# Kernel optimization log

Measured on AMD Instinct MI355X. Metric: run time of the kernel, lower is better.

## Reference

```python
import jax, jax.numpy as jnp
import numpy as np

N_NODES = 200000
N_FRAGS = 50000
N_EDGES = 400000
HDIM = 128
VOCAB = 800


def setup_inputs() -> dict:
    key = jax.random.key(0)
    ks = jax.random.split(key, 9)
    x = jax.random.normal(ks[0], (N_NODES, HDIM), dtype=jnp.float32)
    fragments = jax.random.uniform(ks[1], (N_FRAGS, VOCAB), dtype=jnp.float32)
    emb_table = jax.random.normal(ks[2], (VOCAB, HDIM), dtype=jnp.float32)
    W_f = jax.random.normal(ks[3], (HDIM, HDIM), dtype=jnp.float32) / np.sqrt(HDIM)
    b_f = jax.random.normal(ks[4], (HDIM,), dtype=jnp.float32) * 0.01
    W_s = jax.random.normal(ks[5], (2 * HDIM, HDIM), dtype=jnp.float32) / np.sqrt(2 * HDIM)
    b_s = jax.random.normal(ks[6], (HDIM,), dtype=jnp.float32) * 0.01
    row = jax.random.randint(ks[7], (N_EDGES,), 0, N_NODES, dtype=jnp.int32)
    col = jax.random.randint(ks[8], (N_EDGES,), 0, N_FRAGS, dtype=jnp.int32)
    return {"x": x, "fragments": fragments, "emb_table": emb_table,
            "W_f": W_f, "b_f": b_f, "W_s": W_s, "b_s": b_s,
            "row": row, "col": col}


def _scatter_mean(vals, idx, num_segments):
    s = jax.ops.segment_sum(vals, idx, num_segments=num_segments)
    cnt = jax.ops.segment_sum(jnp.ones((vals.shape[0], 1), vals.dtype), idx,
                              num_segments=num_segments)
    return s / jnp.maximum(cnt, 1.0)


def reference(x, fragments, emb_table, W_f, b_f, W_s, b_s, row, col):
    N, H = x.shape
    F = fragments.shape[0]
    # gather node feats along memberships, mean-pool per fragment: [F, H]
    substructure_x = _scatter_mean(x[row], col, F)
    # fragment type embedding branch
    frag_ids = jnp.argmax(fragments, axis=1)            # [F]
    fragments_emb = emb_table[frag_ids] @ W_f + b_f      # [F, H]
    substructure_x = jnp.concatenate([substructure_x, fragments_emb], axis=1)  # [F, 2H]
    fragment_emb = substructure_x @ W_s + b_s            # [F, H]
    # gather fragment embeddings back to memberships, mean-pool per node: [N, H]
    return _scatter_mean(fragment_emb[col], row, N)
```

## Files before the change

### kernel.cpp

```cpp
#include <hip/hip_runtime.h>

#define HDIM 128
#define VOCAB 800
#define FB 16
#define NB 64
#define TILE 1024
#define TILE_N 512

typedef float f4 __attribute__((ext_vector_type(4)));

#define ACCB(a, h) { \
    a.x += __uint_as_float(h.x << 16); \
    a.y += __uint_as_float(h.x & 0xffff0000u); \
    a.z += __uint_as_float(h.y << 16); \
    a.w += __uint_as_float(h.y & 0xffff0000u); }

static __device__ __forceinline__ unsigned short f2bf(float f) {
    unsigned int u = __float_as_uint(f);
    return (unsigned short)((u + 0x7fffu + ((u >> 16) & 1u)) >> 16);
}

__global__ void k_prep(const float* __restrict__ emb, const float* __restrict__ W_f,
                       const float* __restrict__ W_s, const float* __restrict__ b_f,
                       const float* __restrict__ b_s, float* __restrict__ E2,
                       float* __restrict__ bfs) {
    __shared__ float e[HDIM], t1[HDIM];
    int j = threadIdx.x;
    int v = blockIdx.x;
    if (v < VOCAB) {
        e[j] = emb[(size_t)v * HDIM + j];
        __syncthreads();
        float a = 0.f;
        for (int k = 0; k < HDIM; ++k)
            a = fmaf(e[k], W_f[k * HDIM + j], a);
        t1[j] = a;
        __syncthreads();
        float b = 0.f;
        for (int k = 0; k < HDIM; ++k)
            b = fmaf(t1[k], W_s[(HDIM + k) * HDIM + j], b);
        E2[(size_t)v * HDIM + j] = b;
    } else {
        e[j] = b_f[j];
        __syncthreads();
        float b = b_s[j];
        for (int k = 0; k < HDIM; ++k)
            b = fmaf(e[k], W_s[(HDIM + k) * HDIM + j], b);
        bfs[j] = b;
    }
}

__global__ void k_amc(const float* __restrict__ frags, int* __restrict__ frag_id,
                      const float* __restrict__ x, unsigned short* __restrict__ xb,
                      const int* __restrict__ row, const int* __restrict__ col,
                      int* __restrict__ cntr, int* __restrict__ cntc) {
    int b = blockIdx.x, t = threadIdx.x;
    if (b < 12500) {
        int wave = b * 4 + (t >> 6);
        int lane = t & 63;
        const f4* r = reinterpret_cast<const f4*>(frags + (size_t)wave * VOCAB);
        float best = -1e30f;
        int bidx = 0;
        for (int i = lane; i < VOCAB / 4; i += 64) {
            f4 v = __builtin_nontemporal_load(r + i);
            int base = i * 4;
            if (v.x > best) { best = v.x; bidx = base + 0; }
            if (v.y > best) { best = v.y; bidx = base + 1; }
            if (v.z > best) { best = v.z; bidx = base + 2; }
            if (v.w > best) { best = v.w; bidx = base + 3; }
        }
        for (int off = 32; off > 0; off >>= 1) {
            float ov = __shfl_xor(best, off, 64);
            int   oi = __shfl_xor(bidx, off, 64);
            if (ov > best || (ov == best && oi < bidx)) { best = ov; bidx = oi; }
        }
        if (lane == 0) frag_id[wave] = bidx;
    } else if (b < 12891) {
        int i = (b - 12500) * 256 + t;
        if (i < 100000) {
            int4 r4 = reinterpret_cast<const int4*>(row)[i];
            int4 c4 = reinterpret_cast<const int4*>(col)[i];
            atomicAdd(&cntr[r4.x], 1); atomicAdd(&cntr[r4.y], 1);
            atomicAdd(&cntr[r4.z], 1); atomicAdd(&cntr[r4.w], 1);
            atomicAdd(&cntc[c4.x], 1); atomicAdd(&cntc[c4.y], 1);
            atomicAdd(&cntc[c4.z], 1); atomicAdd(&cntc[c4.w], 1);
        }
    } else {
        size_t i = (size_t)(b - 12891) * 256 + t;
        const f4* xp = reinterpret_cast<const f4*>(x);
        f4 v0 = __builtin_nontemporal_load(xp + 2 * i);
        f4 v1 = __builtin_nontemporal_load(xp + 2 * i + 1);
        uint4 o;
        o.x = (unsigned)f2bf(v0.x) | ((unsigned)f2bf(v0.y) << 16);
        o.y = (unsigned)f2bf(v0.z) | ((unsigned)f2bf(v0.w) << 16);
        o.z = (unsigned)f2bf(v1.x) | ((unsigned)f2bf(v1.y) << 16);
        o.w = (unsigned)f2bf(v1.z) | ((unsigned)f2bf(v1.w) << 16);
        *reinterpret_cast<uint4*>(xb + i * 8) = o;
    }
}

__global__ void k_bsum2(const int* __restrict__ cntc, const int* __restrict__ cntr,
                        int* __restrict__ bsc, int* __restrict__ bsr, int NBC, int F, int N) {
    __shared__ int s[256];
    int t = threadIdx.x;
    const int* cnt;
    int* bsum;
    int bb, L;
    if ((int)blockIdx.x < NBC) { cnt = cntc; bsum = bsc; bb = blockIdx.x; L = F; }
    else                       { cnt = cntr; bsum = bsr; bb = blockIdx.x - NBC; L = N; }
    int i = bb * 256 + t;
    s[t] = (i < L) ? cnt[i] : 0;
    __syncthreads();
    for (int o = 128; o > 0; o >>= 1) {
        if (t < o) s[t] += s[t + o];
        __syncthreads();
    }
    if (t == 0) bsum[bb] = s[0];
}

__global__ void k_scan2(int* __restrict__ bsc, int* __restrict__ bsr, int nbc, int nbr) {
    __shared__ int s[1024];
    int* bsum = (blockIdx.x == 0) ? bsc : bsr;
    int nb    = (blockIdx.x == 0) ? nbc : nbr;
    int t = threadIdx.x;
    int v = (t < nb) ? bsum[t] : 0;
    s[t] = v;
    __syncthreads();
    for (int o = 1; o < 1024; o <<= 1) {
        int a = (t >= o) ? s[t - o] : 0;
        __syncthreads();
        s[t] += a;
        __syncthreads();
    }
    if (t < nb) bsum[t] = s[t] - v;
}

__global__ void k_base2(const int* __restrict__ cntc, const int* __restrict__ cntr,
                        const int* __restrict__ bsc, const int* __restrict__ bsr,
                        int* __restrict__ basec, int* __restrict__ baser,
                        int NBC, int F, int N) {
    __shared__ int s[256];
    int t = threadIdx.x;
    const int *cnt, *bsum;
    int* base;
    int bb, L;
    if ((int)blockIdx.x < NBC) { cnt = cntc; bsum = bsc; base = basec; bb = blockIdx.x; L = F; }
    else                       { cnt = cntr; bsum = bsr; base = baser; bb = blockIdx.x - NBC; L = N; }
    int i = bb * 256 + t;
    int v = (i < L) ? cnt[i] : 0;
    s[t] = v;
    __syncthreads();
    for (int o = 1; o < 256; o <<= 1) {
        int a = (t >= o) ? s[t - o] : 0;
        __syncthreads();
        s[t] += a;
        __syncthreads();
    }
    if (i < L) base[i] = bsum[bb] + s[t] - v;
}

__global__ void k_place(const int* __restrict__ row, const int* __restrict__ col,
                        int* __restrict__ basec, int* __restrict__ baser,
                        int* __restrict__ payc, int* __restrict__ payr, int E) {
    int e = blockIdx.x * 256 + threadIdx.x;
    if (e >= E) return;
    int r = row[e], c = col[e];
    int pc = atomicAdd(&basec[c], 1);
    payc[pc] = r;
    int pr = atomicAdd(&baser[r], 1);
    payr[pr] = c;
}

__global__ __launch_bounds__(256) void k_frag(
        const unsigned short* __restrict__ xb, const int* __restrict__ basec,
        const int* __restrict__ payc, const int* __restrict__ frag_id,
        const float* __restrict__ W_s, const float* __restrict__ E2,
        const float* __restrict__ bfs, unsigned short* __restrict__ fembb) {
    __shared__ float s[FB][HDIM];
    __shared__ int eidx[TILE];
    __shared__ int cb[FB + 1];
    int t = threadIdx.x;
    int g = t >> 5, l = t & 31;
    int fb = blockIdx.x * FB;
    if (t <= FB) {
        int idx = fb + t - 1;
        cb[t] = (idx < 0) ? 0 : basec[idx];
    }
    __syncthreads();
    int st0 = cb[g],     d0 = cb[g + 1] - cb[g];
    int st1 = cb[8 + g], d1 = cb[9 + g] - cb[8 + g];
    int p0 = cb[0], pend = cb[FB];
    const uint2* x2 = reinterpret_cast<const uint2*>(xb);
    float4 a0A = make_float4(0.f, 0.f, 0.f, 0.f), a0B = a0A, a1A = a0A, a1B = a0A;
    for (int tb = p0; tb < pend; tb += TILE) {
        int nload = min(TILE, pend - tb);
        for (int i = t; i < nload; i += 256) eidx[i] = payc[tb + i];
        __syncthreads();
        int lim = tb + nload;
        int lo0 = max(st0, tb) - tb, hi0 = min(st0 + d0, lim) - tb;
        int lo1 = max(st1, tb) - tb, hi1 = min(st1 + d1, lim) - tb;
        int m = max(hi0 - lo0, hi1 - lo1);
        for (int j = 0; j < m; j += 2) {
            if (lo0 + j < hi0)     { uint2 h = x2[(size_t)eidx[lo0 + j]     * 32 + l]; ACCB(a0A, h); }
            if (lo0 + j + 1 < hi0) { uint2 h = x2[(size_t)eidx[lo0 + j + 1] * 32 + l]; ACCB(a0B, h); }
            if (lo1 + j < hi1)     { uint2 h = x2[(size_t)eidx[lo1 + j]     * 32 + l]; ACCB(a1A, h); }
            if (lo1 + j + 1 < hi1) { uint2 h = x2[(size_t)eidx[lo1 + j + 1] * 32 + l]; ACCB(a1B, h); }
        }
        __syncthreads();
    }
    float inv0 = 1.0f / fmaxf((float)d0, 1.0f);
    float inv1 = 1.0f / fmaxf((float)d1, 1.0f);
    float4 r0, r1;
    r0.x = (a0A.x + a0B.x) * inv0; r0.y = (a0A.y + a0B.y) * inv0;
    r0.z = (a0A.z + a0B.z) * inv0; r0.w = (a0A.w + a0B.w) * inv0;
    r1.x = (a1A.x + a1B.x) * inv1; r1.y = (a1A.y + a1B.y) * inv1;
    r1.z = (a1A.z + a1B.z) * inv1; r1.w = (a1A.w + a1B.w) * inv1;
    *reinterpret_cast<float4*>(&s[g][l * 4]) = r0;
    *reinterpret_cast<float4*>(&s[8 + g][l * 4]) = r1;
    __syncthreads();
    int d = t & 127;
    int fh = t >> 7;
    float bv = bfs[d];
    float acc[8];
#pragma unroll
    for (int f = 0; f < 8; ++f)
        acc[f] = E2[(size_t)frag_id[fb + fh * 8 + f] * HDIM + d] + bv;
    for (int k = 0; k < HDIM; k += 4) {
        float w0 = W_s[(k + 0) * HDIM + d];
        float w1 = W_s[(k + 1) * HDIM + d];
        float w2 = W_s[(k + 2) * HDIM + d];
        float w3 = W_s[(k + 3) * HDIM + d];
#pragma unroll
        for (int f = 0; f < 8; ++f) {
            const float4 sv = *reinterpret_cast<const float4*>(&s[fh * 8 + f][k]);
            acc[f] = fmaf(sv.x, w0, acc[f]);
            acc[f] = fmaf(sv.y, w1, acc[f]);
            acc[f] = fmaf(sv.z, w2, acc[f]);
            acc[f] = fmaf(sv.w, w3, acc[f]);
        }
    }
#pragma unroll
    for (int f = 0; f < 8; ++f)
        fembb[(size_t)(fb + fh * 8 + f) * HDIM + d] = f2bf(acc[f]);
}

__global__ __launch_bounds__(256) void k_node(
        const unsigned short* __restrict__ fembb, const int* __restrict__ baser,
        const int* __restrict__ payr, float* __restrict__ out, int N) {
    __shared__ int eidx[TILE_N];
    __shared__ int cb[NB + 1];
    int t = threadIdx.x;
    int g = t >> 5, l = t & 31;
    int n0 = blockIdx.x * NB;
    if (t <= NB) {
        int idx = n0 + t - 1;
        cb[t] = (idx < 0) ? 0 : baser[idx];
    }
    __syncthreads();
    int st_[8], dg_[8];
    float4 a[8];
#pragma unroll
    for (int i = 0; i < 8; ++i) {
        st_[i] = cb[g * 8 + i];
        dg_[i] = cb[g * 8 + i + 1] - st_[i];
        a[i] = make_float4(0.f, 0.f, 0.f, 0.f);
    }
    int p0 = cb[0], pend = cb[NB];
    const uint2* f2p = reinterpret_cast<const uint2*>(fembb);
    for (int tb = p0; tb < pend; tb += TILE_N) {
        int nload = min(TILE_N, pend - tb);
        for (int i = t; i < nload; i += 256) eidx[i] = payr[tb + i];
        __syncthreads();
        int lim = tb + nload;
        int lo[8], hi[8];
        int m = 0;
#pragma unroll
        for (int i = 0; i < 8; ++i) {
            lo[i] = max(st_[i], tb) - tb;
            hi[i] = min(st_[i] + dg_[i], lim) - tb;
            m = max(m, hi[i] - lo[i]);
        }
        for (int j = 0; j < m; ++j) {
#pragma unroll
            for (int i = 0; i < 8; ++i) {
                if (lo[i] + j < hi[i]) {
                    uint2 h = f2p[(size_t)eidx[lo[i] + j] * 32 + l];
                    ACCB(a[i], h);
                }
            }
        }
        __syncthreads();
    }
    f4* o4 = reinterpret_cast<f4*>(out);
#pragma unroll
    for (int i = 0; i < 8; ++i) {
        float inv = 1.0f / fmaxf((float)dg_[i], 1.0f);
        f4 v;
        v.x = a[i].x * inv; v.y = a[i].y * inv;
        v.z = a[i].z * inv; v.w = a[i].w * inv;
        __builtin_nontemporal_store(v, o4 + (size_t)(n0 + g * 8 + i) * 32 + l);
    }
}

extern "C" void kernel_launch(void* const* d_in, const int* in_sizes, int n_in,
                              void* d_out, int out_size, void* d_ws, size_t ws_size,
                              hipStream_t stream) {
    const float* x         = (const float*)d_in[0];
    const float* fragments = (const float*)d_in[1];
    const float* emb_table = (const float*)d_in[2];
    const float* W_f       = (const float*)d_in[3];
    const float* b_f       = (const float*)d_in[4];
    const float* W_s       = (const float*)d_in[5];
    const float* b_s       = (const float*)d_in[6];
    const int*   row       = (const int*)d_in[7];
    const int*   col       = (const int*)d_in[8];
    float* out = (float*)d_out;

    const int N = 200000, F = 50000, E = 400000;
    const int NBC = (F + 255) / 256;
    const int NBR = (N + 255) / 256;

    unsigned short* xb = (unsigned short*)d_out;

    unsigned short* fembb = (unsigned short*)d_ws;
    int* cntc    = (int*)(fembb + (size_t)F * HDIM);
    int* cntr    = cntc + F;
    int* basec   = cntr + N;
    int* baser   = basec + F;
    int* bsc     = baser + N;
    int* bsr     = bsc + 1024;
    int* payc    = bsr + 1024;
    int* payr    = payc + E;
    int* frag_id = payr + E;
    float* E2    = (float*)(frag_id + F);
    float* bfs   = E2 + VOCAB * HDIM;

    hipMemsetAsync(cntc, 0, (size_t)(F + N) * sizeof(int), stream);

    k_amc<<<12891 + 12500, 256, 0, stream>>>(fragments, frag_id, x, xb, row, col, cntr, cntc);
    k_bsum2<<<NBC + NBR, 256, 0, stream>>>(cntc, cntr, bsc, bsr, NBC, F, N);
    k_scan2<<<2, 1024, 0, stream>>>(bsc, bsr, NBC, NBR);
    k_base2<<<NBC + NBR, 256, 0, stream>>>(cntc, cntr, bsc, bsr, basec, baser, NBC, F, N);
    k_place<<<(E + 255) / 256, 256, 0, stream>>>(row, col, basec, baser, payc, payr, E);
    k_prep<<<VOCAB + 1, HDIM, 0, stream>>>(emb_table, W_f, W_s, b_f, b_s, E2, bfs);
    k_frag<<<F / FB, 256, 0, stream>>>(xb, basec, payc, frag_id, W_s, E2, bfs, fembb);
    k_node<<<N / NB, 256, 0, stream>>>(fembb, baser, payr, out, N);
}
```

Before: 251.0 us.

## Merge CSR builds into one scan, fuse prep into k_amc, widen fragment blocks

Concatenates the column and row count/base/payload arrays so one bsum/scan/base chain serves both CSR builds. It folds the embedding-prep matmuls into the tail blocks of k_amc and vectorizes k_place to int4 loads. It also doubles the fragments per block in k_frag, packing fragment pairs into float2 shared memory for the dense projection. The goal is fewer launches and better W_s reuse, at the cost of more registers per thread and fewer k_frag blocks.

```diff
diff --git a/kernel.cpp b/kernel.cpp
--- a/kernel.cpp
+++ b/kernel.cpp
@@ -2,12 +2,13 @@
 
 #define HDIM 128
 #define VOCAB 800
-#define FB 16
+#define FB 32
 #define NB 64
 #define TILE 1024
 #define TILE_N 512
 
 typedef float f4 __attribute__((ext_vector_type(4)));
+typedef float f2 __attribute__((ext_vector_type(2)));
 
 #define ACCB(a, h) { \
     a.x += __uint_as_float(h.x << 16); \
@@ -20,39 +21,15 @@
     return (unsigned short)((u + 0x7fffu + ((u >> 16) & 1u)) >> 16);
 }
 
-__global__ void k_prep(const float* __restrict__ emb, const float* __restrict__ W_f,
-                       const float* __restrict__ W_s, const float* __restrict__ b_f,
-                       const float* __restrict__ b_s, float* __restrict__ E2,
-                       float* __restrict__ bfs) {
-    __shared__ float e[HDIM], t1[HDIM];
-    int j = threadIdx.x;
-    int v = blockIdx.x;
-    if (v < VOCAB) {
-        e[j] = emb[(size_t)v * HDIM + j];
-        __syncthreads();
-        float a = 0.f;
-        for (int k = 0; k < HDIM; ++k)
-            a = fmaf(e[k], W_f[k * HDIM + j], a);
-        t1[j] = a;
-        __syncthreads();
-        float b = 0.f;
-        for (int k = 0; k < HDIM; ++k)
-            b = fmaf(t1[k], W_s[(HDIM + k) * HDIM + j], b);
-        E2[(size_t)v * HDIM + j] = b;
-    } else {
-        e[j] = b_f[j];
-        __syncthreads();
-        float b = b_s[j];
-        for (int k = 0; k < HDIM; ++k)
-            b = fmaf(e[k], W_s[(HDIM + k) * HDIM + j], b);
-        bfs[j] = b;
-    }
-}
-
 __global__ void k_amc(const float* __restrict__ frags, int* __restrict__ frag_id,
                       const float* __restrict__ x, unsigned short* __restrict__ xb,
                       const int* __restrict__ row, const int* __restrict__ col,
-                      int* __restrict__ cntr, int* __restrict__ cntc) {
+                      int* __restrict__ cnt,
+                      const float* __restrict__ emb, const float* __restrict__ W_f,
+                      const float* __restrict__ W_s, const float* __restrict__ b_f,
+                      const float* __restrict__ b_s, float* __restrict__ E2,
+                      float* __restrict__ bfs, int F) {
+    __shared__ float e[2][HDIM], t1[2][HDIM];
     int b = blockIdx.x, t = threadIdx.x;
     if (b < 12500) {
         int wave = b * 4 + (t >> 6);
@@ -79,12 +56,12 @@
         if (i < 100000) {
             int4 r4 = reinterpret_cast<const int4*>(row)[i];
             int4 c4 = reinterpret_cast<const int4*>(col)[i];
-            atomicAdd(&cntr[r4.x], 1); atomicAdd(&cntr[r4.y], 1);
-            atomicAdd(&cntr[r4.z], 1); atomicAdd(&cntr[r4.w], 1);
-            atomicAdd(&cntc[c4.x], 1); atomicAdd(&cntc[c4.y], 1);
-            atomicAdd(&cntc[c4.z], 1); atomicAdd(&cntc[c4.w], 1);
-        }
-    } else {
+            atomicAdd(&cnt[F + r4.x], 1); atomicAdd(&cnt[F + r4.y], 1);
+            atomicAdd(&cnt[F + r4.z], 1); atomicAdd(&cnt[F + r4.w], 1);
+            atomicAdd(&cnt[c4.x], 1); atomicAdd(&cnt[c4.y], 1);
+            atomicAdd(&cnt[c4.z], 1); atomicAdd(&cnt[c4.w], 1);
+        }
+    } else if (b < 25391) {
         size_t i = (size_t)(b - 12891) * 256 + t;
         const f4* xp = reinterpret_cast<const f4*>(x);
         f4 v0 = __builtin_nontemporal_load(xp + 2 * i);
@@ -95,32 +72,50 @@
         o.z = (unsigned)f2bf(v1.x) | ((unsigned)f2bf(v1.y) << 16);
         o.w = (unsigned)f2bf(v1.z) | ((unsigned)f2bf(v1.w) << 16);
         *reinterpret_cast<uint4*>(xb + i * 8) = o;
-    }
-}
-
-__global__ void k_bsum2(const int* __restrict__ cntc, const int* __restrict__ cntr,
-                        int* __restrict__ bsc, int* __restrict__ bsr, int NBC, int F, int N) {
+    } else {
+        int bp = b - 25391;
+        int j = t & 127, half = t >> 7;
+        if (bp < 400) {
+            int v = bp * 2 + half;
+            e[half][j] = emb[(size_t)v * HDIM + j];
+            __syncthreads();
+            float a = 0.f;
+            for (int k = 0; k < HDIM; ++k)
+                a = fmaf(e[half][k], W_f[k * HDIM + j], a);
+            t1[half][j] = a;
+            __syncthreads();
+            float bb = 0.f;
+            for (int k = 0; k < HDIM; ++k)
+                bb = fmaf(t1[half][k], W_s[(HDIM + k) * HDIM + j], bb);
+            E2[(size_t)v * HDIM + j] = bb;
+        } else {
+            if (half == 0) e[0][j] = b_f[j];
+            __syncthreads();
+            if (half == 0) {
+                float bb = b_s[j];
+                for (int k = 0; k < HDIM; ++k)
+                    bb = fmaf(e[0][k], W_s[(HDIM + k) * HDIM + j], bb);
+                bfs[j] = bb;
+            }
+        }
+    }
+}
+
+__global__ void k_bsum(const int* __restrict__ cnt, int L, int* __restrict__ bsum) {
     __shared__ int s[256];
     int t = threadIdx.x;
-    const int* cnt;
-    int* bsum;
-    int bb, L;
-    if ((int)blockIdx.x < NBC) { cnt = cntc; bsum = bsc; bb = blockIdx.x; L = F; }
-    else                       { cnt = cntr; bsum = bsr; bb = blockIdx.x - NBC; L = N; }
-    int i = bb * 256 + t;
+    int i = blockIdx.x * 256 + t;
     s[t] = (i < L) ? cnt[i] : 0;
     __syncthreads();
     for (int o = 128; o > 0; o >>= 1) {
         if (t < o) s[t] += s[t + o];
         __syncthreads();
     }
-    if (t == 0) bsum[bb] = s[0];
-}
-
-__global__ void k_scan2(int* __restrict__ bsc, int* __restrict__ bsr, int nbc, int nbr) {
+    if (t == 0) bsum[blockIdx.x] = s[0];
+}
+
+__global__ void k_scan(int* __restrict__ bsum, int nb) {
     __shared__ int s[1024];
-    int* bsum = (blockIdx.x == 0) ? bsc : bsr;
-    int nb    = (blockIdx.x == 0) ? nbc : nbr;
     int t = threadIdx.x;
     int v = (t < nb) ? bsum[t] : 0;
     s[t] = v;
@@ -134,18 +129,11 @@
     if (t < nb) bsum[t] = s[t] - v;
 }
 
-__global__ void k_base2(const int* __restrict__ cntc, const int* __restrict__ cntr,
-                        const int* __restrict__ bsc, const int* __restrict__ bsr,
-                        int* __restrict__ basec, int* __restrict__ baser,
-                        int NBC, int F, int N) {
+__global__ void k_base(const int* __restrict__ cnt, const int* __restrict__ bsum, int L,
+                       int* __restrict__ base) {
     __shared__ int s[256];
     int t = threadIdx.x;
-    const int *cnt, *bsum;
-    int* base;
-    int bb, L;
-    if ((int)blockIdx.x < NBC) { cnt = cntc; bsum = bsc; base = basec; bb = blockIdx.x; L = F; }
-    else                       { cnt = cntr; bsum = bsr; base = baser; bb = blockIdx.x - NBC; L = N; }
-    int i = bb * 256 + t;
+    int i = blockIdx.x * 256 + t;
     int v = (i < L) ? cnt[i] : 0;
     s[t] = v;
     __syncthreads();
@@ -155,27 +143,28 @@
         s[t] += a;
         __syncthreads();
     }
-    if (i < L) base[i] = bsum[bb] + s[t] - v;
+    if (i < L) base[i] = bsum[blockIdx.x] + s[t] - v;
 }
 
 __global__ void k_place(const int* __restrict__ row, const int* __restrict__ col,
-                        int* __restrict__ basec, int* __restrict__ baser,
-                        int* __restrict__ payc, int* __restrict__ payr, int E) {
-    int e = blockIdx.x * 256 + threadIdx.x;
-    if (e >= E) return;
-    int r = row[e], c = col[e];
-    int pc = atomicAdd(&basec[c], 1);
-    payc[pc] = r;
-    int pr = atomicAdd(&baser[r], 1);
-    payr[pr] = c;
+                        int* __restrict__ base, int* __restrict__ pay, int F, int E) {
+    int i = blockIdx.x * 256 + threadIdx.x;
+    if (i >= E / 4) return;
+    int4 r4 = reinterpret_cast<const int4*>(row)[i];
+    int4 c4 = reinterpret_cast<const int4*>(col)[i];
+#define PL(r, c) { \
+    int pc = atomicAdd(&base[c], 1); pay[pc] = r; \
+    int pr = atomicAdd(&base[F + r], 1); pay[pr] = c; }
+    PL(r4.x, c4.x) PL(r4.y, c4.y) PL(r4.z, c4.z) PL(r4.w, c4.w)
+#undef PL
 }
 
 __global__ __launch_bounds__(256) void k_frag(
-        const unsigned short* __restrict__ xb, const int* __restrict__ basec,
-        const int* __restrict__ payc, const int* __restrict__ frag_id,
+        const unsigned short* __restrict__ xb, const int* __restrict__ base,
+        const int* __restrict__ pay, const int* __restrict__ frag_id,
         const float* __restrict__ W_s, const float* __restrict__ E2,
-        const float* __restrict__ bfs, unsigned short* __restrict__ fembb) {
-    __shared__ float s[FB][HDIM];
+        const float* __restrict__ bfs, unsigned short* __restrict__ fembb, int F, int E) {
+    __shared__ f2 sI[FB / 2][HDIM];
     __shared__ int eidx[TILE];
     __shared__ int cb[FB + 1];
     int t = threadIdx.x;
@@ -183,69 +172,99 @@
     int fb = blockIdx.x * FB;
     if (t <= FB) {
         int idx = fb + t - 1;
-        cb[t] = (idx < 0) ? 0 : basec[idx];
-    }
-    __syncthreads();
-    int st0 = cb[g],     d0 = cb[g + 1] - cb[g];
-    int st1 = cb[8 + g], d1 = cb[9 + g] - cb[8 + g];
+        cb[t] = (idx < 0) ? 0 : ((idx < F) ? base[idx] : E);
+    }
+    __syncthreads();
+    int fr[4], st[4], dg[4];
+#pragma unroll
+    for (int q = 0; q < 4; ++q) {
+        fr[q] = q * 8 + g;
+        st[q] = cb[fr[q]];
+        dg[q] = cb[fr[q] + 1] - st[q];
+    }
     int p0 = cb[0], pend = cb[FB];
     const uint2* x2 = reinterpret_cast<const uint2*>(xb);
-    float4 a0A = make_float4(0.f, 0.f, 0.f, 0.f), a0B = a0A, a1A = a0A, a1B = a0A;
+    float4 aA[4], aB[4];
+#pragma unroll
+    for (int q = 0; q < 4; ++q) {
+        aA[q] = make_float4(0.f, 0.f, 0.f, 0.f);
+        aB[q] = aA[q];
+    }
     for (int tb = p0; tb < pend; tb += TILE) {
         int nload = min(TILE, pend - tb);
-        for (int i = t; i < nload; i += 256) eidx[i] = payc[tb + i];
+        for (int i = t; i < nload; i += 256) eidx[i] = pay[tb + i];
         __syncthreads();
         int lim = tb + nload;
-        int lo0 = max(st0, tb) - tb, hi0 = min(st0 + d0, lim) - tb;
-        int lo1 = max(st1, tb) - tb, hi1 = min(st1 + d1, lim) - tb;
-        int m = max(hi0 - lo0, hi1 - lo1);
+        int lo[4], hi[4], m = 0;
+#pragma unroll
+        for (int q = 0; q < 4; ++q) {
+            lo[q] = max(st[q], tb) - tb;
+            hi[q] = min(st[q] + dg[q], lim) - tb;
+            m = max(m, hi[q] - lo[q]);
+        }
         for (int j = 0; j < m; j += 2) {
-            if (lo0 + j < hi0)     { uint2 h = x2[(size_t)eidx[lo0 + j]     * 32 + l]; ACCB(a0A, h); }
-            if (lo0 + j + 1 < hi0) { uint2 h = x2[(size_t)eidx[lo0 + j + 1] * 32 + l]; ACCB(a0B, h); }
-            if (lo1 + j < hi1)     { uint2 h = x2[(size_t)eidx[lo1 + j]     * 32 + l]; ACCB(a1A, h); }
-            if (lo1 + j + 1 < hi1) { uint2 h = x2[(size_t)eidx[lo1 + j + 1] * 32 + l]; ACCB(a1B, h); }
-        }
-        __syncthreads();
-    }
-    float inv0 = 1.0f / fmaxf((float)d0, 1.0f);
-    float inv1 = 1.0f / fmaxf((float)d1, 1.0f);
-    float4 r0, r1;
-    r0.x = (a0A.x + a0B.x) * inv0; r0.y = (a0A.y + a0B.y) * inv0;
-    r0.z = (a0A.z + a0B.z) * inv0; r0.w = (a0A.w + a0B.w) * inv0;
-    r1.x = (a1A.x + a1B.x) * inv1; r1.y = (a1A.y + a1B.y) * inv1;
-    r1.z = (a1A.z + a1B.z) * inv1; r1.w = (a1A.w + a1B.w) * inv1;
-    *reinterpret_cast<float4*>(&s[g][l * 4]) = r0;
-    *reinterpret_cast<float4*>(&s[8 + g][l * 4]) = r1;
+#pragma unroll
+            for (int q = 0; q < 4; ++q) {
+                if (lo[q] + j < hi[q])     { uint2 h = x2[(size_t)eidx[lo[q] + j]     * 32 + l]; ACCB(aA[q], h); }
+                if (lo[q] + j + 1 < hi[q]) { uint2 h = x2[(size_t)eidx[lo[q] + j + 1] * 32 + l]; ACCB(aB[q], h); }
+            }
+        }
+        __syncthreads();
+    }
+#pragma unroll
+    for (int q = 0; q < 4; ++q) {
+        float inv = 1.0f / fmaxf((float)dg[q], 1.0f);
+        float4 r;
+        r.x = (aA[q].x + aB[q].x) * inv; r.y = (aA[q].y + aB[q].y) * inv;
+        r.z = (aA[q].z + aB[q].z) * inv; r.w = (aA[q].w + aB[q].w) * inv;
+        int pr = fr[q] >> 1, pa = fr[q] & 1;
+        if (pa == 0) {
+            sI[pr][l * 4 + 0].x = r.x; sI[pr][l * 4 + 1].x = r.y;
+            sI[pr][l * 4 + 2].x = r.z; sI[pr][l * 4 + 3].x = r.w;
+        } else {
+            sI[pr][l * 4 + 0].y = r.x; sI[pr][l * 4 + 1].y = r.y;
+            sI[pr][l * 4 + 2].y = r.z; sI[pr][l * 4 + 3].y = r.w;
+        }
+    }
     __syncthreads();
     int d = t & 127;
     int fh = t >> 7;
     float bv = bfs[d];
-    float acc[8];
-#pragma unroll
-    for (int f = 0; f < 8; ++f)
-        acc[f] = E2[(size_t)frag_id[fb + fh * 8 + f] * HDIM + d] + bv;
-    for (int k = 0; k < HDIM; k += 4) {
+    f2 acc2[8];
+#pragma unroll
+    for (int q = 0; q < 8; ++q) {
+        int pr = fh * 8 + q;
+        int fA = fb + 2 * pr, fB = fA + 1;
+        int idA = frag_id[min(fA, F - 1)];
+        int idB = frag_id[min(fB, F - 1)];
+        acc2[q].x = E2[(size_t)idA * HDIM + d] + bv;
+        acc2[q].y = E2[(size_t)idB * HDIM + d] + bv;
+    }
+    for (int k = 0; k < HDIM; k += 2) {
         float w0 = W_s[(k + 0) * HDIM + d];
         float w1 = W_s[(k + 1) * HDIM + d];
-        float w2 = W_s[(k + 2) * HDIM + d];
-        float w3 = W_s[(k + 3) * HDIM + d];
-#pragma unroll
-        for (int f = 0; f < 8; ++f) {
-            const float4 sv = *reinterpret_cast<const float4*>(&s[fh * 8 + f][k]);
-            acc[f] = fmaf(sv.x, w0, acc[f]);
-            acc[f] = fmaf(sv.y, w1, acc[f]);
-            acc[f] = fmaf(sv.z, w2, acc[f]);
-            acc[f] = fmaf(sv.w, w3, acc[f]);
-        }
-    }
-#pragma unroll
-    for (int f = 0; f < 8; ++f)
-        fembb[(size_t)(fb + fh * 8 + f) * HDIM + d] = f2bf(acc[f]);
+        f2 w0v; w0v.x = w0; w0v.y = w0;
+        f2 w1v; w1v.x = w1; w1v.y = w1;
+#pragma unroll
+        for (int q = 0; q < 8; ++q) {
+            int pr = fh * 8 + q;
+            f2 v0 = sI[pr][k];
+            f2 v1 = sI[pr][k + 1];
+            acc2[q] += v0 * w0v + v1 * w1v;
+        }
+    }
+#pragma unroll
+    for (int q = 0; q < 8; ++q) {
+        int pr = fh * 8 + q;
+        int fA = fb + 2 * pr;
+        if (fA < F)     fembb[(size_t)fA * HDIM + d]       = f2bf(acc2[q].x);
+        if (fA + 1 < F) fembb[(size_t)(fA + 1) * HDIM + d] = f2bf(acc2[q].y);
+    }
 }
 
 __global__ __launch_bounds__(256) void k_node(
-        const unsigned short* __restrict__ fembb, const int* __restrict__ baser,
-        const int* __restrict__ payr, float* __restrict__ out, int N) {
+        const unsigned short* __restrict__ fembb, const int* __restrict__ base,
+        const int* __restrict__ pay, float* __restrict__ out, int F, int E, int N) {
     __shared__ int eidx[TILE_N];
     __shared__ int cb[NB + 1];
     int t = threadIdx.x;
@@ -253,7 +272,7 @@
     int n0 = blockIdx.x * NB;
     if (t <= NB) {
         int idx = n0 + t - 1;
-        cb[t] = (idx < 0) ? 0 : baser[idx];
+        cb[t] = (idx < 0) ? E : base[F + idx];
     }
     __syncthreads();
     int st_[8], dg_[8];
@@ -268,7 +287,7 @@
     const uint2* f2p = reinterpret_cast<const uint2*>(fembb);
     for (int tb = p0; tb < pend; tb += TILE_N) {
         int nload = min(TILE_N, pend - tb);
-        for (int i = t; i < nload; i += 256) eidx[i] = payr[tb + i];
+        for (int i = t; i < nload; i += 256) eidx[i] = pay[tb + i];
         __syncthreads();
         int lim = tb + nload;
         int lo[8], hi[8];
@@ -316,32 +335,29 @@
     float* out = (float*)d_out;
 
     const int N = 200000, F = 50000, E = 400000;
-    const int NBC = (F + 255) / 256;
-    const int NBR = (N + 255) / 256;
+    const int L = F + N;
+    const int NBT = (L + 255) / 256;
 
     unsigned short* xb = (unsigned short*)d_out;
 
     unsigned short* fembb = (unsigned short*)d_ws;
-    int* cntc    = (int*)(fembb + (size_t)F * HDIM);
-    int* cntr    = cntc + F;
-    int* basec   = cntr + N;
-    int* baser   = basec + F;
-    int* bsc     = baser + N;
-    int* bsr     = bsc + 1024;
-    int* payc    = bsr + 1024;
-    int* payr    = payc + E;
-    int* frag_id = payr + E;
+    int* cnt     = (int*)(fembb + (size_t)F * HDIM);
+    int* base    = cnt + L;
+    int* bsum    = base + L;
+    int* pay     = bsum + 1024;
+    int* frag_id = pay + 2 * E;
     float* E2    = (float*)(frag_id + F);
     float* bfs   = E2 + VOCAB * HDIM;
 
-    hipMemsetAsync(cntc, 0, (size_t)(F + N) * sizeof(int), stream);
-
-    k_amc<<<12891 + 12500, 256, 0, stream>>>(fragments, frag_id, x, xb, row, col, cntr, cntc);
-    k_bsum2<<<NBC + NBR, 256, 0, stream>>>(cntc, cntr, bsc, bsr, NBC, F, N);
-    k_scan2<<<2, 1024, 0, stream>>>(bsc, bsr, NBC, NBR);
-    k_base2<<<NBC + NBR, 256, 0, stream>>>(cntc, cntr, bsc, bsr, basec, baser, NBC, F, N);
-    k_place<<<(E + 255) / 256, 256, 0, stream>>>(row, col, basec, baser, payc, payr, E);
-    k_prep<<<VOCAB + 1, HDIM, 0, stream>>>(emb_table, W_f, W_s, b_f, b_s, E2, bfs);
-    k_frag<<<F / FB, 256, 0, stream>>>(xb, basec, payc, frag_id, W_s, E2, bfs, fembb);
-    k_node<<<N / NB, 256, 0, stream>>>(fembb, baser, payr, out, N);
-}
+    hipMemsetAsync(cnt, 0, (size_t)L * sizeof(int), stream);
+
+    k_amc<<<25792, 256, 0, stream>>>(fragments, frag_id, x, xb, row, col, cnt,
+                                     emb_table, W_f, W_s, b_f, b_s, E2, bfs, F);
+    k_bsum<<<NBT, 256, 0, stream>>>(cnt, L, bsum);
+    k_scan<<<1, 1024, 0, stream>>>(bsum, NBT);
+    k_base<<<NBT, 256, 0, stream>>>(cnt, bsum, L, base);
+    k_place<<<(E / 4 + 255) / 256, 256, 0, stream>>>(row, col, base, pay, F, E);
+    k_frag<<<(F + FB - 1) / FB, 256, 0, stream>>>(xb, base, pay, frag_id, W_s, E2, bfs,
+                                                  fembb, F, E);
+    k_node<<<N / NB, 256, 0, stream>>>(fembb, base, pay, out, F, E, N);
+}
```

New measurement: 250.1 us. About the same (-0.4%).
